# Optimization experiments

Measured on AMD Instinct MI355X. Metric: run time of the kernel, lower is better.

## Reference

```python
import jax, jax.numpy as jnp
import numpy as np

E, D, I, T = 8, 4096, 1024, 32768  # experts, model dim, dim//4, total packed tokens


def setup_inputs() -> dict:
    key = jax.random.key(0)
    k1, k2, k3, k4 = jax.random.split(key, 4)
    x = jax.random.normal(k1, (T, D), dtype=jnp.float32)
    # trunc_normal(std=0.02) approximated by scaled normal for the reference
    w1 = jax.random.normal(k2, (E, D, I), dtype=jnp.float32) * 0.02
    w2 = jax.random.normal(k3, (E, I, D), dtype=jnp.float32) * 0.02
    w3 = jax.random.normal(k4, (E, D, I), dtype=jnp.float32) * 0.02
    # tokens split evenly across experts; sum == T
    num_tokens_per_expert = jnp.full((E,), T // E, dtype=jnp.int32)
    return {"x": x, "w1": w1, "w2": w2, "w3": w3,
            "num_tokens_per_expert": num_tokens_per_expert}


def reference(x, w1, w2, w3, num_tokens_per_expert):
    # bf16 compute, cast back to input dtype (matches ops.gmm path in torch code)
    g = num_tokens_per_expert.astype(jnp.int32)
    xb = x.astype(jnp.bfloat16)
    w1b = w1.astype(jnp.bfloat16)
    w2b = w2.astype(jnp.bfloat16)
    w3b = w3.astype(jnp.bfloat16)
    # grouped GEMM: rows of x are grouped by expert per g
    x1 = jax.lax.ragged_dot(xb, w1b, g)          # [T, I]
    x3 = jax.lax.ragged_dot(xb, w3b, g)          # [T, I]
    h = jax.nn.silu(x1) * x3                      # SwiGLU
    out = jax.lax.ragged_dot(h, w2b, g)           # [T, D]
    return out.astype(x.dtype)
```

## Files before the change

### kernel.cpp

```cpp
#include <hip/hip_runtime.h>
#include <hip/hip_bf16.h>

typedef __attribute__((ext_vector_type(8))) short bf16x8;
typedef __attribute__((ext_vector_type(4))) float f32x4;

#define SBAR() __builtin_amdgcn_sched_barrier(0)
#define WBAR() __builtin_amdgcn_s_barrier()
#define VMC4() asm volatile("s_waitcnt vmcnt(4)" ::: "memory")
#define VMC0() asm volatile("s_waitcnt vmcnt(0)" ::: "memory")

__device__ __forceinline__ ushort f2bf(float f) {
  union { float f; unsigned u; } v; v.f = f;
  unsigned r = v.u + 0x7fffu + ((v.u >> 16) & 1u);
  return (ushort)(r >> 16);
}

__device__ __forceinline__ void gld_lds16(const ushort* gsrc, ushort* lds) {
  __builtin_amdgcn_global_load_lds((const __attribute__((address_space(1))) void*)gsrc,
                                   (__attribute__((address_space(3))) void*)lds, 16, 0, 0);
}

__device__ __forceinline__ f32x4 MF(bf16x8 a, bf16x8 b, f32x4 c) {
  return __builtin_amdgcn_mfma_f32_16x16x32_bf16(a, b, c, 0, 0, 0);
}

__device__ __forceinline__ void xcd_map(int bid, int CT, int& r, int& c) {
  const int xcd = bid & 7, j = bid >> 3;
  r = xcd + 8 * (j / CT);
  c = j % CT;
}

__device__ __forceinline__ int expert_of(const int* g, int E, int m0) {
  int e = 0, base = 0;
  while (e < E - 1 && m0 >= base + g[e]) { base += g[e]; ++e; }
  return e;
}

__global__ __launch_bounds__(256) void k_pack_x(
    const float* __restrict__ x, ushort* __restrict__ xb, int D) {
  __shared__ ushort sm[256][66];
  const int kt = blockIdx.x;
  const int rt = blockIdx.y;
  const int t = threadIdx.x;
  const int c0 = kt * 64;
  const size_t r0 = (size_t)rt * 256;
#pragma unroll
  for (int p = 0; p < 16; ++p) {
    const int row = p * 16 + (t >> 4);
    const float4 v = *reinterpret_cast<const float4*>(x + (r0 + row) * D + c0 + (t & 15) * 4);
    ushort4 u; u.x = f2bf(v.x); u.y = f2bf(v.y); u.z = f2bf(v.z); u.w = f2bf(v.w);
    *reinterpret_cast<ushort4*>(&sm[row][(t & 15) * 4]) = u;
  }
  __syncthreads();
  ushort* outp = xb + ((size_t)rt * (D >> 6) + kt) * 16384;
#pragma unroll
  for (int p = 0; p < 8; ++p) {
    ushort u[8];
#pragma unroll
    for (int j = 0; j < 8; ++j) u[j] = sm[t][p * 8 + j];
    *reinterpret_cast<uint4*>(outp + p * 2048 + t * 8) = *reinterpret_cast<uint4*>(u);
  }
}

__global__ __launch_bounds__(256) void k_pack_w(
    const float* __restrict__ w, ushort* __restrict__ wp, int R, int C, int rbShift) {
  __shared__ ushort sm[64][66];
  const int e = blockIdx.z;
  const size_t mat = (size_t)R * C;
  const float* s = w + (size_t)e * mat;
  ushort* d = wp + (size_t)e * mat;
  const int c0 = blockIdx.x * 64;
  const int r0 = blockIdx.y * 64;
  const int t = threadIdx.x;
#pragma unroll
  for (int p = 0; p < 4; ++p) {
    const int r = p * 16 + (t >> 4);
    const float4 v = *reinterpret_cast<const float4*>(s + (size_t)(r0 + r) * C + c0 + (t & 15) * 4);
    ushort4 u; u.x = f2bf(v.x); u.y = f2bf(v.y); u.z = f2bf(v.z); u.w = f2bf(v.w);
    *reinterpret_cast<ushort4*>(&sm[r][(t & 15) * 4]) = u;
  }
  __syncthreads();
  const int RB = 1 << rbShift;
  const size_t tilebase = ((size_t)(c0 >> rbShift) * (R >> 6) + (r0 >> 6)) * ((size_t)RB * 64);
  const int nbase = c0 & (RB - 1);
#pragma unroll
  for (int p = 0; p < 2; ++p) {
    const int uu = p * 256 + t;
    const int kc = uu >> 6;
    const int rr = uu & 63;
    ushort u[8];
#pragma unroll
    for (int j = 0; j < 8; ++j) u[j] = sm[kc * 8 + j][rr];
    *reinterpret_cast<uint4*>(d + tilebase + (size_t)kc * (RB * 8) + (size_t)(nbase + rr) * 8) =
        *reinterpret_cast<uint4*>(u);
  }
}

__global__ __launch_bounds__(512, 2) void k_gemm1_8p(
    const ushort* __restrict__ xb, const ushort* __restrict__ w1p,
    const ushort* __restrict__ w3p, const int* __restrict__ g,
    ushort* __restrict__ h, int T, int D, int I, int E) {
  __shared__ ushort lds[2][32768];

  const int CT = I >> 7;
  int r, c; xcd_map(blockIdx.x, CT, r, c);
  const int m0 = r << 8, n0 = c << 7;
  const int e = expert_of(g, E, m0);

  const int tid = threadIdx.x;
  const int lane = tid & 63, wave = tid >> 6;
  const int wr = wave >> 2, wc = wave & 3;
  const int l15 = lane & 15, l16 = lane >> 4;

  const int KT = D >> 6;
  const ushort* pA  = xb  + (size_t)r * (D >> 6) * 16384;
  const ushort* pB1 = w1p + (size_t)e * I * D + (size_t)c * (D >> 6) * 8192;
  const ushort* pB3 = w3p + (size_t)e * I * D + (size_t)c * (D >> 6) * 8192;

  const int sto = tid * 8;
  const int aoff  = l16 * 2048 + (wr * 128 + l15) * 8;
  const int b1off = 16384 + l16 * 1024 + (wc * 32 + l15) * 8;
  const int b3off = b1off + 8192;

  const f32x4 zero = {0.f, 0.f, 0.f, 0.f};
  f32x4 acc1[8][2], acc3[8][2];
#pragma unroll
  for (int mi = 0; mi < 8; ++mi)
#pragma unroll
    for (int ni = 0; ni < 2; ++ni) { acc1[mi][ni] = zero; acc3[mi][ni] = zero; }

  {
    ushort* L = lds[0];
    gld_lds16(pA + sto,          L + sto);
    gld_lds16(pA + 4096 + sto,   L + 4096 + sto);
    gld_lds16(pB1 + sto,         L + 16384 + sto);
    gld_lds16(pB3 + sto,         L + 24576 + sto);
    gld_lds16(pA + 8192 + sto,   L + 8192 + sto);
    gld_lds16(pA + 12288 + sto,  L + 12288 + sto);
    gld_lds16(pB1 + 4096 + sto,  L + 20480 + sto);
    gld_lds16(pB3 + 4096 + sto,  L + 28672 + sto);
  }
  VMC4(); WBAR(); SBAR();

  for (int t = 0; t < KT; ++t) {
    ushort* B = lds[t & 1];
    ushort* N = lds[(t + 1) & 1];
    const bool pf = (t + 1 < KT);
    const ushort* nA  = pA  + (size_t)(t + 1) * 16384;
    const ushort* nB1 = pB1 + (size_t)(t + 1) * 8192;
    const ushort* nB3 = pB3 + (size_t)(t + 1) * 8192;

    bf16x8 af[4], b1f[2], b3f[2];
    SBAR();
#pragma unroll
    for (int mi = 0; mi < 4; ++mi) af[mi] = *(const bf16x8*)&B[aoff + mi * 128];
    b1f[0] = *(const bf16x8*)&B[b1off];        b1f[1] = *(const bf16x8*)&B[b1off + 128];
    b3f[0] = *(const bf16x8*)&B[b3off];        b3f[1] = *(const bf16x8*)&B[b3off + 128];
    if (pf) { gld_lds16(nA + sto, N + sto); gld_lds16(nA + 4096 + sto, N + 4096 + sto); }
    SBAR(); WBAR(); SBAR();
    __builtin_amdgcn_s_setprio(1);
#pragma unroll
    for (int mi = 0; mi < 4; ++mi)
#pragma unroll
      for (int ni = 0; ni < 2; ++ni) {
        acc1[mi][ni] = MF(af[mi], b1f[ni], acc1[mi][ni]);
        acc3[mi][ni] = MF(af[mi], b3f[ni], acc3[mi][ni]);
      }
    __builtin_amdgcn_s_setprio(0);
    SBAR(); WBAR();
    SBAR();
#pragma unroll
    for (int mi = 0; mi < 4; ++mi) af[mi] = *(const bf16x8*)&B[aoff + (mi + 4) * 128];
    if (pf) { gld_lds16(nB1 + sto, N + 16384 + sto); gld_lds16(nB3 + sto, N + 24576 + sto); }
    SBAR(); WBAR(); SBAR();
    __builtin_amdgcn_s_setprio(1);
#pragma unroll
    for (int mi = 0; mi < 4; ++mi)
#pragma unroll
      for (int ni = 0; ni < 2; ++ni) {
        acc1[mi + 4][ni] = MF(af[mi], b1f[ni], acc1[mi + 4][ni]);
        acc3[mi + 4][ni] = MF(af[mi], b3f[ni], acc3[mi + 4][ni]);
      }
    __builtin_amdgcn_s_setprio(0);
    SBAR();
    if (pf) { VMC4(); } else { VMC0(); }
    WBAR();
    SBAR();
#pragma unroll
    for (int mi = 0; mi < 4; ++mi) af[mi] = *(const bf16x8*)&B[aoff + 8192 + mi * 128];
    b1f[0] = *(const bf16x8*)&B[b1off + 4096];  b1f[1] = *(const bf16x8*)&B[b1off + 4096 + 128];
    b3f[0] = *(const bf16x8*)&B[b3off + 4096];  b3f[1] = *(const bf16x8*)&B[b3off + 4096 + 128];
    if (pf) { gld_lds16(nA + 8192 + sto, N + 8192 + sto);
              gld_lds16(nA + 12288 + sto, N + 12288 + sto); }
    SBAR(); WBAR(); SBAR();
    __builtin_amdgcn_s_setprio(1);
#pragma unroll
    for (int mi = 0; mi < 4; ++mi)
#pragma unroll
      for (int ni = 0; ni < 2; ++ni) {
        acc1[mi][ni] = MF(af[mi], b1f[ni], acc1[mi][ni]);
        acc3[mi][ni] = MF(af[mi], b3f[ni], acc3[mi][ni]);
      }
    __builtin_amdgcn_s_setprio(0);
    SBAR(); WBAR();
    SBAR();
#pragma unroll
    for (int mi = 0; mi < 4; ++mi) af[mi] = *(const bf16x8*)&B[aoff + 8192 + (mi + 4) * 128];
    if (pf) { gld_lds16(nB1 + 4096 + sto, N + 20480 + sto);
              gld_lds16(nB3 + 4096 + sto, N + 28672 + sto); }
    SBAR(); WBAR(); SBAR();
    __builtin_amdgcn_s_setprio(1);
#pragma unroll
    for (int mi = 0; mi < 4; ++mi)
#pragma unroll
      for (int ni = 0; ni < 2; ++ni) {
        acc1[mi + 4][ni] = MF(af[mi], b1f[ni], acc1[mi + 4][ni]);
        acc3[mi + 4][ni] = MF(af[mi], b3f[ni], acc3[mi + 4][ni]);
      }
    __builtin_amdgcn_s_setprio(0);
    SBAR();
    VMC4();
    WBAR();
  }

#pragma unroll
  for (int mi = 0; mi < 8; ++mi)
#pragma unroll
    for (int ni = 0; ni < 2; ++ni)
#pragma unroll
      for (int rr = 0; rr < 4; ++rr) {
        const float v1 = acc1[mi][ni][rr];
        const float v3 = acc3[mi][ni][rr];
        const float sv = v1 / (1.f + __expf(-v1));
        const int row = m0 + wr * 128 + mi * 16 + l16 * 4 + rr;
        const int col = n0 + wc * 32 + ni * 16 + l15;
        const size_t off = ((size_t)(row >> 8) * (I >> 6) + (col >> 6)) * 16384 +
                           ((col >> 3) & 7) * 2048 + (row & 255) * 8 + (col & 7);
        h[off] = f2bf(sv * v3);
      }
}

__global__ __launch_bounds__(512, 2) void k_gemm2_8p(
    const ushort* __restrict__ h, const ushort* __restrict__ w2p,
    const int* __restrict__ g, float* __restrict__ out,
    int T, int D, int I, int E) {
  __shared__ ushort lds[2][32768];

  const int CT = D >> 8;
  int r, cb; xcd_map(blockIdx.x, CT, r, cb);
  const int m0 = r << 8, n0 = cb << 8;
  const int e = expert_of(g, E, m0);

  const int tid = threadIdx.x;
  const int lane = tid & 63, wave = tid >> 6;
  const int wr = wave >> 2, wc = wave & 3;
  const int l15 = lane & 15, l16 = lane >> 4;

  const int KT = I >> 6;
  const ushort* pA = h   + (size_t)r * (I >> 6) * 16384;
  const ushort* pB = w2p + (size_t)e * D * I + (size_t)cb * (I >> 6) * 16384;

  const int sto = tid * 8;
  const int aoff = l16 * 2048 + (wr * 128 + l15) * 8;
  const int boff = 16384 + l16 * 2048 + (wc * 64 + l15) * 8;

  const f32x4 zero = {0.f, 0.f, 0.f, 0.f};
  f32x4 acc[8][4];
#pragma unroll
  for (int mi = 0; mi < 8; ++mi)
#pragma unroll
    for (int ni = 0; ni < 4; ++ni) acc[mi][ni] = zero;

  {
    ushort* L = lds[0];
    gld_lds16(pA + sto,          L + sto);
    gld_lds16(pA + 4096 + sto,   L + 4096 + sto);
    gld_lds16(pB + sto,          L + 16384 + sto);
    gld_lds16(pB + 4096 + sto,   L + 20480 + sto);
    gld_lds16(pA + 8192 + sto,   L + 8192 + sto);
    gld_lds16(pA + 12288 + sto,  L + 12288 + sto);
    gld_lds16(pB + 8192 + sto,   L + 24576 + sto);
    gld_lds16(pB + 12288 + sto,  L + 28672 + sto);
  }
  VMC4(); WBAR(); SBAR();

  for (int t = 0; t < KT; ++t) {
    ushort* B = lds[t & 1];
    ushort* N = lds[(t + 1) & 1];
    const bool pf = (t + 1 < KT);
    const ushort* nA = pA + (size_t)(t + 1) * 16384;
    const ushort* nB = pB + (size_t)(t + 1) * 16384;

    bf16x8 af[4], bf[4];
    SBAR();
#pragma unroll
    for (int mi = 0; mi < 4; ++mi) af[mi] = *(const bf16x8*)&B[aoff + mi * 128];
#pragma unroll
    for (int ni = 0; ni < 4; ++ni) bf[ni] = *(const bf16x8*)&B[boff + ni * 128];
    if (pf) { gld_lds16(nA + sto, N + sto); gld_lds16(nA + 4096 + sto, N + 4096 + sto); }
    SBAR(); WBAR(); SBAR();
    __builtin_amdgcn_s_setprio(1);
#pragma unroll
    for (int mi = 0; mi < 4; ++mi)
#pragma unroll
      for (int ni = 0; ni < 4; ++ni) acc[mi][ni] = MF(af[mi], bf[ni], acc[mi][ni]);
    __builtin_amdgcn_s_setprio(0);
    SBAR(); WBAR();
    SBAR();
#pragma unroll
    for (int mi = 0; mi < 4; ++mi) af[mi] = *(const bf16x8*)&B[aoff + (mi + 4) * 128];
    if (pf) { gld_lds16(nB + sto, N + 16384 + sto); gld_lds16(nB + 4096 + sto, N + 20480 + sto); }
    SBAR(); WBAR(); SBAR();
    __builtin_amdgcn_s_setprio(1);
#pragma unroll
    for (int mi = 0; mi < 4; ++mi)
#pragma unroll
      for (int ni = 0; ni < 4; ++ni) acc[mi + 4][ni] = MF(af[mi], bf[ni], acc[mi + 4][ni]);
    __builtin_amdgcn_s_setprio(0);
    SBAR();
    if (pf) { VMC4(); } else { VMC0(); }
    WBAR();
    SBAR();
#pragma unroll
    for (int mi = 0; mi < 4; ++mi) af[mi] = *(const bf16x8*)&B[aoff + 8192 + mi * 128];
#pragma unroll
    for (int ni = 0; ni < 4; ++ni) bf[ni] = *(const bf16x8*)&B[boff + 8192 + ni * 128];
    if (pf) { gld_lds16(nA + 8192 + sto, N + 8192 + sto);
              gld_lds16(nA + 12288 + sto, N + 12288 + sto); }
    SBAR(); WBAR(); SBAR();
    __builtin_amdgcn_s_setprio(1);
#pragma unroll
    for (int mi = 0; mi < 4; ++mi)
#pragma unroll
      for (int ni = 0; ni < 4; ++ni) acc[mi][ni] = MF(af[mi], bf[ni], acc[mi][ni]);
    __builtin_amdgcn_s_setprio(0);
    SBAR(); WBAR();
    SBAR();
#pragma unroll
    for (int mi = 0; mi < 4; ++mi) af[mi] = *(const bf16x8*)&B[aoff + 8192 + (mi + 4) * 128];
    if (pf) { gld_lds16(nB + 8192 + sto, N + 24576 + sto);
              gld_lds16(nB + 12288 + sto, N + 28672 + sto); }
    SBAR(); WBAR(); SBAR();
    __builtin_amdgcn_s_setprio(1);
#pragma unroll
    for (int mi = 0; mi < 4; ++mi)
#pragma unroll
      for (int ni = 0; ni < 4; ++ni) acc[mi + 4][ni] = MF(af[mi], bf[ni], acc[mi + 4][ni]);
    __builtin_amdgcn_s_setprio(0);
    SBAR();
    VMC4();
    WBAR();
  }

#pragma unroll
  for (int mi = 0; mi < 8; ++mi)
#pragma unroll
    for (int ni = 0; ni < 4; ++ni)
#pragma unroll
      for (int rr = 0; rr < 4; ++rr) {
        const int row = m0 + wr * 128 + mi * 16 + l16 * 4 + rr;
        const int col = n0 + wc * 64 + ni * 16 + l15;
        out[(size_t)row * D + col] = acc[mi][ni][rr];
      }
}

extern "C" void kernel_launch(void* const* d_in, const int* in_sizes, int n_in,
                              void* d_out, int out_size, void* d_ws, size_t ws_size,
                              hipStream_t stream) {
  const float* x  = (const float*)d_in[0];
  const float* w1 = (const float*)d_in[1];
  const float* w2 = (const float*)d_in[2];
  const float* w3 = (const float*)d_in[3];
  const int*   g  = (const int*)d_in[4];

  const int E = in_sizes[4];
  const int D = 4096;
  const int I = 1024;
  const int T = in_sizes[0] / D;

  const size_t szW = (size_t)E * D * I * sizeof(ushort);
  const size_t szH = (size_t)T * I * sizeof(ushort);
  const size_t szX = (size_t)T * D * sizeof(ushort);
  const size_t need = 2 * szW + szH + szX;
  if (ws_size < need) return;

  char* ws = (char*)d_ws;
  ushort* w1p = (ushort*)ws;
  ushort* w3p = (ushort*)(ws + szW);
  ushort* h   = (ushort*)(ws + 2 * szW);
  ushort* xb  = (ushort*)(ws + 2 * szW + szH);
  ushort* w2p = w1p;

  float* out = (float*)d_out;

  k_pack_w<<<dim3(I / 64, D / 64, E), 256, 0, stream>>>(w1, w1p, D, I, 7);
  k_pack_w<<<dim3(I / 64, D / 64, E), 256, 0, stream>>>(w3, w3p, D, I, 7);
  k_pack_x<<<dim3(D / 64, T / 256), 256, 0, stream>>>(x, xb, D);

  k_gemm1_8p<<<dim3((T / 256) * (I / 128)), 512, 0, stream>>>(xb, w1p, w3p, g, h, T, D, I, E);

  k_pack_w<<<dim3(D / 64, I / 64, E), 256, 0, stream>>>(w2, w2p, I, D, 8);

  k_gemm2_8p<<<dim3((T / 256) * (D / 256)), 512, 0, stream>>>(h, w2p, g, out, T, D, I, E);
}
```

Baseline: 1.056 ms.

## Deepen GEMM prefetch to two tiles ahead with in-place half-buffer refill

```diff
diff --git a/kernel.cpp b/kernel.cpp
--- a/kernel.cpp
+++ b/kernel.cpp
@@ -6,8 +6,13 @@
 
 #define SBAR() __builtin_amdgcn_sched_barrier(0)
 #define WBAR() __builtin_amdgcn_s_barrier()
-#define VMC4() asm volatile("s_waitcnt vmcnt(4)" ::: "memory")
-#define VMC0() asm volatile("s_waitcnt vmcnt(0)" ::: "memory")
+
+template<int N> __device__ __forceinline__ void vmcw() {
+  if constexpr (N >= 12)     asm volatile("s_waitcnt vmcnt(12)" ::: "memory");
+  else if constexpr (N == 8) asm volatile("s_waitcnt vmcnt(8)" ::: "memory");
+  else if constexpr (N == 4) asm volatile("s_waitcnt vmcnt(4)" ::: "memory");
+  else                       asm volatile("s_waitcnt vmcnt(0)" ::: "memory");
+}
 
 __device__ __forceinline__ ushort f2bf(float f) {
   union { float f; unsigned u; } v; v.f = f;
@@ -96,6 +101,90 @@
   }
 }
 
+template<bool PF, int C1, int C2>
+__device__ __forceinline__ void g1_tile(
+    ushort* B, const ushort* nA, const ushort* nB1, const ushort* nB3,
+    int sto, int aoff, int b1off, int b3off,
+    f32x4 (&acc1)[8][2], f32x4 (&acc3)[8][2]) {
+  bf16x8 af[4], b1f[2], b3f[2];
+  SBAR();
+#pragma unroll
+  for (int mi = 0; mi < 4; ++mi) af[mi] = *(const bf16x8*)&B[aoff + mi * 128];
+  b1f[0] = *(const bf16x8*)&B[b1off];       b1f[1] = *(const bf16x8*)&B[b1off + 128];
+  b3f[0] = *(const bf16x8*)&B[b3off];       b3f[1] = *(const bf16x8*)&B[b3off + 128];
+  SBAR(); WBAR(); SBAR();
+  __builtin_amdgcn_s_setprio(1);
+#pragma unroll
+  for (int mi = 0; mi < 4; ++mi)
+#pragma unroll
+    for (int ni = 0; ni < 2; ++ni) {
+      acc1[mi][ni] = MF(af[mi], b1f[ni], acc1[mi][ni]);
+      acc3[mi][ni] = MF(af[mi], b3f[ni], acc3[mi][ni]);
+    }
+  __builtin_amdgcn_s_setprio(0);
+  SBAR(); WBAR();
+  SBAR();
+#pragma unroll
+  for (int mi = 0; mi < 4; ++mi) af[mi] = *(const bf16x8*)&B[aoff + (mi + 4) * 128];
+  SBAR(); WBAR(); SBAR();
+  if (PF) {
+    gld_lds16(nA + sto,         B + sto);
+    gld_lds16(nA + 4096 + sto,  B + 4096 + sto);
+    gld_lds16(nB1 + sto,        B + 16384 + sto);
+    gld_lds16(nB3 + sto,        B + 24576 + sto);
+  }
+  __builtin_amdgcn_s_setprio(1);
+#pragma unroll
+  for (int mi = 0; mi < 4; ++mi)
+#pragma unroll
+    for (int ni = 0; ni < 2; ++ni) {
+      acc1[mi + 4][ni] = MF(af[mi], b1f[ni], acc1[mi + 4][ni]);
+      acc3[mi + 4][ni] = MF(af[mi], b3f[ni], acc3[mi + 4][ni]);
+    }
+  __builtin_amdgcn_s_setprio(0);
+  SBAR();
+  vmcw<C1>();
+  WBAR();
+  SBAR();
+#pragma unroll
+  for (int mi = 0; mi < 4; ++mi) af[mi] = *(const bf16x8*)&B[aoff + 8192 + mi * 128];
+  b1f[0] = *(const bf16x8*)&B[b1off + 4096]; b1f[1] = *(const bf16x8*)&B[b1off + 4096 + 128];
+  b3f[0] = *(const bf16x8*)&B[b3off + 4096]; b3f[1] = *(const bf16x8*)&B[b3off + 4096 + 128];
+  SBAR(); WBAR(); SBAR();
+  __builtin_amdgcn_s_setprio(1);
+#pragma unroll
+  for (int mi = 0; mi < 4; ++mi)
+#pragma unroll
+    for (int ni = 0; ni < 2; ++ni) {
+      acc1[mi][ni] = MF(af[mi], b1f[ni], acc1[mi][ni]);
+      acc3[mi][ni] = MF(af[mi], b3f[ni], acc3[mi][ni]);
+    }
+  __builtin_amdgcn_s_setprio(0);
+  SBAR(); WBAR();
+  SBAR();
+#pragma unroll
+  for (int mi = 0; mi < 4; ++mi) af[mi] = *(const bf16x8*)&B[aoff + 8192 + (mi + 4) * 128];
+  SBAR(); WBAR(); SBAR();
+  if (PF) {
+    gld_lds16(nA + 8192 + sto,   B + 8192 + sto);
+    gld_lds16(nA + 12288 + sto,  B + 12288 + sto);
+    gld_lds16(nB1 + 4096 + sto,  B + 20480 + sto);
+    gld_lds16(nB3 + 4096 + sto,  B + 28672 + sto);
+  }
+  __builtin_amdgcn_s_setprio(1);
+#pragma unroll
+  for (int mi = 0; mi < 4; ++mi)
+#pragma unroll
+    for (int ni = 0; ni < 2; ++ni) {
+      acc1[mi + 4][ni] = MF(af[mi], b1f[ni], acc1[mi + 4][ni]);
+      acc3[mi + 4][ni] = MF(af[mi], b3f[ni], acc3[mi + 4][ni]);
+    }
+  __builtin_amdgcn_s_setprio(0);
+  SBAR();
+  vmcw<C2>();
+  WBAR();
+}
+
 __global__ __launch_bounds__(512, 2) void k_gemm1_8p(
     const ushort* __restrict__ xb, const ushort* __restrict__ w1p,
     const ushort* __restrict__ w3p, const int* __restrict__ g,
@@ -130,98 +219,34 @@
     for (int ni = 0; ni < 2; ++ni) { acc1[mi][ni] = zero; acc3[mi][ni] = zero; }
 
   {
-    ushort* L = lds[0];
-    gld_lds16(pA + sto,          L + sto);
-    gld_lds16(pA + 4096 + sto,   L + 4096 + sto);
-    gld_lds16(pB1 + sto,         L + 16384 + sto);
-    gld_lds16(pB3 + sto,         L + 24576 + sto);
-    gld_lds16(pA + 8192 + sto,   L + 8192 + sto);
-    gld_lds16(pA + 12288 + sto,  L + 12288 + sto);
-    gld_lds16(pB1 + 4096 + sto,  L + 20480 + sto);
-    gld_lds16(pB3 + 4096 + sto,  L + 28672 + sto);
-  }
-  VMC4(); WBAR(); SBAR();
-
-  for (int t = 0; t < KT; ++t) {
-    ushort* B = lds[t & 1];
-    ushort* N = lds[(t + 1) & 1];
-    const bool pf = (t + 1 < KT);
-    const ushort* nA  = pA  + (size_t)(t + 1) * 16384;
-    const ushort* nB1 = pB1 + (size_t)(t + 1) * 8192;
-    const ushort* nB3 = pB3 + (size_t)(t + 1) * 8192;
-
-    bf16x8 af[4], b1f[2], b3f[2];
-    SBAR();
-#pragma unroll
-    for (int mi = 0; mi < 4; ++mi) af[mi] = *(const bf16x8*)&B[aoff + mi * 128];
-    b1f[0] = *(const bf16x8*)&B[b1off];        b1f[1] = *(const bf16x8*)&B[b1off + 128];
-    b3f[0] = *(const bf16x8*)&B[b3off];        b3f[1] = *(const bf16x8*)&B[b3off + 128];
-    if (pf) { gld_lds16(nA + sto, N + sto); gld_lds16(nA + 4096 + sto, N + 4096 + sto); }
-    SBAR(); WBAR(); SBAR();
-    __builtin_amdgcn_s_setprio(1);
-#pragma unroll
-    for (int mi = 0; mi < 4; ++mi)
-#pragma unroll
-      for (int ni = 0; ni < 2; ++ni) {
-        acc1[mi][ni] = MF(af[mi], b1f[ni], acc1[mi][ni]);
-        acc3[mi][ni] = MF(af[mi], b3f[ni], acc3[mi][ni]);
-      }
-    __builtin_amdgcn_s_setprio(0);
-    SBAR(); WBAR();
-    SBAR();
-#pragma unroll
-    for (int mi = 0; mi < 4; ++mi) af[mi] = *(const bf16x8*)&B[aoff + (mi + 4) * 128];
-    if (pf) { gld_lds16(nB1 + sto, N + 16384 + sto); gld_lds16(nB3 + sto, N + 24576 + sto); }
-    SBAR(); WBAR(); SBAR();
-    __builtin_amdgcn_s_setprio(1);
-#pragma unroll
-    for (int mi = 0; mi < 4; ++mi)
-#pragma unroll
-      for (int ni = 0; ni < 2; ++ni) {
-        acc1[mi + 4][ni] = MF(af[mi], b1f[ni], acc1[mi + 4][ni]);
-        acc3[mi + 4][ni] = MF(af[mi], b3f[ni], acc3[mi + 4][ni]);
-      }
-    __builtin_amdgcn_s_setprio(0);
-    SBAR();
-    if (pf) { VMC4(); } else { VMC0(); }
-    WBAR();
-    SBAR();
-#pragma unroll
-    for (int mi = 0; mi < 4; ++mi) af[mi] = *(const bf16x8*)&B[aoff + 8192 + mi * 128];
-    b1f[0] = *(const bf16x8*)&B[b1off + 4096];  b1f[1] = *(const bf16x8*)&B[b1off + 4096 + 128];
-    b3f[0] = *(const bf16x8*)&B[b3off + 4096];  b3f[1] = *(const bf16x8*)&B[b3off + 4096 + 128];
-    if (pf) { gld_lds16(nA + 8192 + sto, N + 8192 + sto);
-              gld_lds16(nA + 12288 + sto, N + 12288 + sto); }
-    SBAR(); WBAR(); SBAR();
-    __builtin_amdgcn_s_setprio(1);
-#pragma unroll
-    for (int mi = 0; mi < 4; ++mi)
-#pragma unroll
-      for (int ni = 0; ni < 2; ++ni) {
-        acc1[mi][ni] = MF(af[mi], b1f[ni], acc1[mi][ni]);
-        acc3[mi][ni] = MF(af[mi], b3f[ni], acc3[mi][ni]);
-      }
-    __builtin_amdgcn_s_setprio(0);
-    SBAR(); WBAR();
-    SBAR();
-#pragma unroll
-    for (int mi = 0; mi < 4; ++mi) af[mi] = *(const bf16x8*)&B[aoff + 8192 + (mi + 4) * 128];
-    if (pf) { gld_lds16(nB1 + 4096 + sto, N + 20480 + sto);
-              gld_lds16(nB3 + 4096 + sto, N + 28672 + sto); }
-    SBAR(); WBAR(); SBAR();
-    __builtin_amdgcn_s_setprio(1);
-#pragma unroll
-    for (int mi = 0; mi < 4; ++mi)
-#pragma unroll
-      for (int ni = 0; ni < 2; ++ni) {
-        acc1[mi + 4][ni] = MF(af[mi], b1f[ni], acc1[mi + 4][ni]);
-        acc3[mi + 4][ni] = MF(af[mi], b3f[ni], acc3[mi + 4][ni]);
-      }
-    __builtin_amdgcn_s_setprio(0);
-    SBAR();
-    VMC4();
-    WBAR();
-  }
+    ushort* L0 = lds[0]; ushort* L1 = lds[1];
+    gld_lds16(pA + sto,          L0 + sto);
+    gld_lds16(pA + 4096 + sto,   L0 + 4096 + sto);
+    gld_lds16(pB1 + sto,         L0 + 16384 + sto);
+    gld_lds16(pB3 + sto,         L0 + 24576 + sto);
+    gld_lds16(pA + 8192 + sto,   L0 + 8192 + sto);
+    gld_lds16(pA + 12288 + sto,  L0 + 12288 + sto);
+    gld_lds16(pB1 + 4096 + sto,  L0 + 20480 + sto);
+    gld_lds16(pB3 + 4096 + sto,  L0 + 28672 + sto);
+    gld_lds16(pA + 16384 + sto,         L1 + sto);
+    gld_lds16(pA + 16384 + 4096 + sto,  L1 + 4096 + sto);
+    gld_lds16(pB1 + 8192 + sto,         L1 + 16384 + sto);
+    gld_lds16(pB3 + 8192 + sto,         L1 + 24576 + sto);
+    gld_lds16(pA + 16384 + 8192 + sto,  L1 + 8192 + sto);
+    gld_lds16(pA + 16384 + 12288 + sto, L1 + 12288 + sto);
+    gld_lds16(pB1 + 8192 + 4096 + sto,  L1 + 20480 + sto);
+    gld_lds16(pB3 + 8192 + 4096 + sto,  L1 + 28672 + sto);
+  }
+  vmcw<12>(); WBAR(); SBAR();
+
+  int t = 0;
+  for (; t < KT - 2; ++t)
+    g1_tile<true, 12, 12>(lds[t & 1], pA + (size_t)(t + 2) * 16384,
+                          pB1 + (size_t)(t + 2) * 8192, pB3 + (size_t)(t + 2) * 8192,
+                          sto, aoff, b1off, b3off, acc1, acc3);
+  g1_tile<false, 8, 4>(lds[t & 1], pA, pB1, pB3, sto, aoff, b1off, b3off, acc1, acc3);
+  ++t;
+  g1_tile<false, 0, 0>(lds[t & 1], pA, pB1, pB3, sto, aoff, b1off, b3off, acc1, acc3);
 
 #pragma unroll
   for (int mi = 0; mi < 8; ++mi)
@@ -240,6 +265,77 @@
       }
 }
 
+template<bool PF, int C1, int C2>
+__device__ __forceinline__ void g2_tile(
+    ushort* B, const ushort* nA, const ushort* nB,
+    int sto, int aoff, int boff, f32x4 (&acc)[8][4]) {
+  bf16x8 af[4], bf[4];
+  SBAR();
+#pragma unroll
+  for (int mi = 0; mi < 4; ++mi) af[mi] = *(const bf16x8*)&B[aoff + mi * 128];
+#pragma unroll
+  for (int ni = 0; ni < 4; ++ni) bf[ni] = *(const bf16x8*)&B[boff + ni * 128];
+  SBAR(); WBAR(); SBAR();
+  __builtin_amdgcn_s_setprio(1);
+#pragma unroll
+  for (int mi = 0; mi < 4; ++mi)
+#pragma unroll
+    for (int ni = 0; ni < 4; ++ni) acc[mi][ni] = MF(af[mi], bf[ni], acc[mi][ni]);
+  __builtin_amdgcn_s_setprio(0);
+  SBAR(); WBAR();
+  SBAR();
+#pragma unroll
+  for (int mi = 0; mi < 4; ++mi) af[mi] = *(const bf16x8*)&B[aoff + (mi + 4) * 128];
+  SBAR(); WBAR(); SBAR();
+  if (PF) {
+    gld_lds16(nA + sto,         B + sto);
+    gld_lds16(nA + 4096 + sto,  B + 4096 + sto);
+    gld_lds16(nB + sto,         B + 16384 + sto);
+    gld_lds16(nB + 4096 + sto,  B + 20480 + sto);
+  }
+  __builtin_amdgcn_s_setprio(1);
+#pragma unroll
+  for (int mi = 0; mi < 4; ++mi)
+#pragma unroll
+    for (int ni = 0; ni < 4; ++ni) acc[mi + 4][ni] = MF(af[mi], bf[ni], acc[mi + 4][ni]);
+  __builtin_amdgcn_s_setprio(0);
+  SBAR();
+  vmcw<C1>();
+  WBAR();
+  SBAR();
+#pragma unroll
+  for (int mi = 0; mi < 4; ++mi) af[mi] = *(const bf16x8*)&B[aoff + 8192 + mi * 128];
+#pragma unroll
+  for (int ni = 0; ni < 4; ++ni) bf[ni] = *(const bf16x8*)&B[boff + 8192 + ni * 128];
+  SBAR(); WBAR(); SBAR();
+  __builtin_amdgcn_s_setprio(1);
+#pragma unroll
+  for (int mi = 0; mi < 4; ++mi)
+#pragma unroll
+    for (int ni = 0; ni < 4; ++ni) acc[mi][ni] = MF(af[mi], bf[ni], acc[mi][ni]);
+  __builtin_amdgcn_s_setprio(0);
+  SBAR(); WBAR();
+  SBAR();
+#pragma unroll
+  for (int mi = 0; mi < 4; ++mi) af[mi] = *(const bf16x8*)&B[aoff + 8192 + (mi + 4) * 128];
+  SBAR(); WBAR(); SBAR();
+  if (PF) {
+    gld_lds16(nA + 8192 + sto,   B + 8192 + sto);
+    gld_lds16(nA + 12288 + sto,  B + 12288 + sto);
+    gld_lds16(nB + 8192 + sto,   B + 24576 + sto);
+    gld_lds16(nB + 12288 + sto,  B + 28672 + sto);
+  }
+  __builtin_amdgcn_s_setprio(1);
+#pragma unroll
+  for (int mi = 0; mi < 4; ++mi)
+#pragma unroll
+    for (int ni = 0; ni < 4; ++ni) acc[mi + 4][ni] = MF(af[mi], bf[ni], acc[mi + 4][ni]);
+  __builtin_amdgcn_s_setprio(0);
+  SBAR();
+  vmcw<C2>();
+  WBAR();
+}
+
 __global__ __launch_bounds__(512, 2) void k_gemm2_8p(
     const ushort* __restrict__ h, const ushort* __restrict__ w2p,
     const int* __restrict__ g, float* __restrict__ out,
@@ -272,85 +368,33 @@
     for (int ni = 0; ni < 4; ++ni) acc[mi][ni] = zero;
 
   {
-    ushort* L = lds[0];
-    gld_lds16(pA + sto,          L + sto);
-    gld_lds16(pA + 4096 + sto,   L + 4096 + sto);
-    gld_lds16(pB + sto,          L + 16384 + sto);
-    gld_lds16(pB + 4096 + sto,   L + 20480 + sto);
-    gld_lds16(pA + 8192 + sto,   L + 8192 + sto);
-    gld_lds16(pA + 12288 + sto,  L + 12288 + sto);
-    gld_lds16(pB + 8192 + sto,   L + 24576 + sto);
-    gld_lds16(pB + 12288 + sto,  L + 28672 + sto);
-  }
-  VMC4(); WBAR(); SBAR();
-
-  for (int t = 0; t < KT; ++t) {
-    ushort* B = lds[t & 1];
-    ushort* N = lds[(t + 1) & 1];
-    const bool pf = (t + 1 < KT);
-    const ushort* nA = pA + (size_t)(t + 1) * 16384;
-    const ushort* nB = pB + (size_t)(t + 1) * 16384;
-
-    bf16x8 af[4], bf[4];
-    SBAR();
-#pragma unroll
-    for (int mi = 0; mi < 4; ++mi) af[mi] = *(const bf16x8*)&B[aoff + mi * 128];
-#pragma unroll
-    for (int ni = 0; ni < 4; ++ni) bf[ni] = *(const bf16x8*)&B[boff + ni * 128];
-    if (pf) { gld_lds16(nA + sto, N + sto); gld_lds16(nA + 4096 + sto, N + 4096 + sto); }
-    SBAR(); WBAR(); SBAR();
-    __builtin_amdgcn_s_setprio(1);
-#pragma unroll
-    for (int mi = 0; mi < 4; ++mi)
-#pragma unroll
-      for (int ni = 0; ni < 4; ++ni) acc[mi][ni] = MF(af[mi], bf[ni], acc[mi][ni]);
-    __builtin_amdgcn_s_setprio(0);
-    SBAR(); WBAR();
-    SBAR();
-#pragma unroll
-    for (int mi = 0; mi < 4; ++mi) af[mi] = *(const bf16x8*)&B[aoff + (mi + 4) * 128];
-    if (pf) { gld_lds16(nB + sto, N + 16384 + sto); gld_lds16(nB + 4096 + sto, N + 20480 + sto); }
-    SBAR(); WBAR(); SBAR();
-    __builtin_amdgcn_s_setprio(1);
-#pragma unroll
-    for (int mi = 0; mi < 4; ++mi)
-#pragma unroll
-      for (int ni = 0; ni < 4; ++ni) acc[mi + 4][ni] = MF(af[mi], bf[ni], acc[mi + 4][ni]);
-    __builtin_amdgcn_s_setprio(0);
-    SBAR();
-    if (pf) { VMC4(); } else { VMC0(); }
-    WBAR();
-    SBAR();
-#pragma unroll
-    for (int mi = 0; mi < 4; ++mi) af[mi] = *(const bf16x8*)&B[aoff + 8192 + mi * 128];
-#pragma unroll
-    for (int ni = 0; ni < 4; ++ni) bf[ni] = *(const bf16x8*)&B[boff + 8192 + ni * 128];
-    if (pf) { gld_lds16(nA + 8192 + sto, N + 8192 + sto);
-              gld_lds16(nA + 12288 + sto, N + 12288 + sto); }
-    SBAR(); WBAR(); SBAR();
-    __builtin_amdgcn_s_setprio(1);
-#pragma unroll
-    for (int mi = 0; mi < 4; ++mi)
-#pragma unroll
-      for (int ni = 0; ni < 4; ++ni) acc[mi][ni] = MF(af[mi], bf[ni], acc[mi][ni]);
-    __builtin_amdgcn_s_setprio(0);
-    SBAR(); WBAR();
-    SBAR();
-#pragma unroll
-    for (int mi = 0; mi < 4; ++mi) af[mi] = *(const bf16x8*)&B[aoff + 8192 + (mi + 4) * 128];
-    if (pf) { gld_lds16(nB + 8192 + sto, N + 24576 + sto);
-              gld_lds16(nB + 12288 + sto, N + 28672 + sto); }
-    SBAR(); WBAR(); SBAR();
-    __builtin_amdgcn_s_setprio(1);
-#pragma unroll
-    for (int mi = 0; mi < 4; ++mi)
-#pragma unroll
-      for (int ni = 0; ni < 4; ++ni) acc[mi + 4][ni] = MF(af[mi], bf[ni], acc[mi + 4][ni]);
-    __builtin_amdgcn_s_setprio(0);
-    SBAR();
-    VMC4();
-    WBAR();
-  }
+    ushort* L0 = lds[0]; ushort* L1 = lds[1];
+    gld_lds16(pA + sto,          L0 + sto);
+    gld_lds16(pA + 4096 + sto,   L0 + 4096 + sto);
+    gld_lds16(pB + sto,          L0 + 16384 + sto);
+    gld_lds16(pB + 4096 + sto,   L0 + 20480 + sto);
+    gld_lds16(pA + 8192 + sto,   L0 + 8192 + sto);
+    gld_lds16(pA + 12288 + sto,  L0 + 12288 + sto);
+    gld_lds16(pB + 8192 + sto,   L0 + 24576 + sto);
+    gld_lds16(pB + 12288 + sto,  L0 + 28672 + sto);
+    gld_lds16(pA + 16384 + sto,          L1 + sto);
+    gld_lds16(pA + 16384 + 4096 + sto,   L1 + 4096 + sto);
+    gld_lds16(pB + 16384 + sto,          L1 + 16384 + sto);
+    gld_lds16(pB + 16384 + 4096 + sto,   L1 + 20480 + sto);
+    gld_lds16(pA + 16384 + 8192 + sto,   L1 + 8192 + sto);
+    gld_lds16(pA + 16384 + 12288 + sto,  L1 + 12288 + sto);
+    gld_lds16(pB + 16384 + 8192 + sto,   L1 + 24576 + sto);
+    gld_lds16(pB + 16384 + 12288 + sto,  L1 + 28672 + sto);
+  }
+  vmcw<12>(); WBAR(); SBAR();
+
+  int t = 0;
+  for (; t < KT - 2; ++t)
+    g2_tile<true, 12, 12>(lds[t & 1], pA + (size_t)(t + 2) * 16384,
+                          pB + (size_t)(t + 2) * 16384, sto, aoff, boff, acc);
+  g2_tile<false, 8, 4>(lds[t & 1], pA, pB, sto, aoff, boff, acc);
+  ++t;
+  g2_tile<false, 0, 0>(lds[t & 1], pA, pB, sto, aoff, boff, acc);
 
 #pragma unroll
   for (int mi = 0; mi < 8; ++mi)
```

Measured after the change: 1.053 ms. Within noise of the previous version (-0.3%).
